# Performance work log

Hardware: AMD Instinct MI355X
Metric: run time of the kernel (lower is better)

Reference implementation:

```python
import jax, jax.numpy as jnp
import numpy as np

B, C, H, W = 64, 32, 112, 112
RANK = 3


def setup_inputs() -> dict:
    key = jax.random.key(0)
    k1, k2, k3, k4, k5 = jax.random.split(key, 5)
    N = H * W  # 12544
    return {
        "x": jax.random.uniform(k1, (B, C, H, W), dtype=jnp.float32),
        "p_buffer": jax.random.normal(k2, (B, N, RANK), dtype=jnp.float32),
        "q_buffer": jax.random.normal(k3, (B, C, RANK), dtype=jnp.float32),
        "grad_p_buffer": jax.random.normal(k4, (B, N, RANK), dtype=jnp.float32),
        "grad_q_buffer": jax.random.normal(k5, (B, C, RANK), dtype=jnp.float32),
        "n_iter": 2,
    }


def _power_svd(X, P, Q, n_iter):
    # X: [b, c, n]; P: [b, n, r]; Q: [b, c, r]
    for i in range(n_iter):
        if i == n_iter - 1:
            P = jnp.linalg.qr(P)[0]  # batched reduced QR, tall-skinny (n x r)
        Q = jnp.einsum('bcn,bnr->bcr', X, P)
        if i == n_iter - 1:
            Q = jnp.linalg.qr(Q)[0]  # batched reduced QR (c x r)
        P = jnp.einsum('bcn,bcr->bnr', X, Q)  # X^T @ Q
    return P, Q


def reference(x, p_buffer, q_buffer, grad_p_buffer, grad_q_buffer, n_iter):
    shape = x.shape
    X = x.reshape(shape[0], shape[1], -1)  # [B, C, H*W]
    P, Q = _power_svd(X, p_buffer, q_buffer, n_iter)
    # low-rank reconstruction Q @ P^T, back to original shape
    return jnp.einsum('bcr,bnr->bcn', Q, P).reshape(shape)
```

## Files before the change

### kernel.cpp

```cpp
#include <hip/hip_runtime.h>
#include <math.h>

#define N_HW 12544
#define TN 128
#define NCH 98
#define KB 16

#define WS_P1 0
#define WS_P2 (64 * KB * 1024)
#define WS_QP (2 * 64 * KB * 1024)
#define WS_U  (WS_QP + 64 * KB * 96)

typedef __attribute__((ext_vector_type(8)))  short short8;
typedef __attribute__((ext_vector_type(16))) float f32x16;
typedef __attribute__((ext_vector_type(4)))  float f32x4;

#define MFMA(a, b, c) __builtin_amdgcn_mfma_f32_32x32x16_bf16((a), (b), (c), 0, 0, 0)

#define LDS_BAR()                                                \
    do {                                                         \
        asm volatile("s_waitcnt lgkmcnt(0)" ::: "memory");       \
        __builtin_amdgcn_s_barrier();                            \
        asm volatile("" ::: "memory");                           \
    } while (0)

__device__ __forceinline__ void split2(float f, ushort& h, ushort& m) {
    unsigned u = __builtin_bit_cast(unsigned, f);
    h = (ushort)(u >> 16);
    float fh = __builtin_bit_cast(float, u & 0xffff0000u);
    float rm = f - fh;
    unsigned um = __builtin_bit_cast(unsigned, rm);
    um += 0x7fffu + ((um >> 16) & 1u);
    m = (ushort)(um >> 16);
}

__device__ __forceinline__ int xq(int c, int o) {
    return c * 16 + ((o & 8) | ((o ^ c) & 7));
}

__global__ __launch_bounds__(256)
void k1_gram(const float* __restrict__ x, const float* __restrict__ p,
             float* __restrict__ P1, float* __restrict__ P2, float* __restrict__ Qp)
{
    const int b = blockIdx.y, kb = blockIdx.x;
    const int tid = threadIdx.x;
    const int lane = tid & 63, wave = tid >> 6;

    __shared__ alignas(16) float SMEM[5120];
    uint4* XS  = (uint4*)SMEM;
    float* dmp = SMEM;
    __shared__ alignas(16) ushort PTH[3 * TN], PTM[3 * TN];

    const int c = tid >> 3, oc = tid & 7;
    const float* xrow = x + ((size_t)b * 32 + c) * N_HW;
    const float* pbat = p + (size_t)b * N_HW * 3;

    f32x16 D1 = {0,0,0,0,0,0,0,0,0,0,0,0,0,0,0,0};
    f32x16 D2 = {0,0,0,0,0,0,0,0,0,0,0,0,0,0,0,0};
    f32x16 DQ = {0,0,0,0,0,0,0,0,0,0,0,0,0,0,0,0};
    const int cl = lane & 31, g = lane >> 5;
    const int rr = (cl < 3) ? cl : 0;

#define LOADX(PX, jj)                                                          \
    do {                                                                       \
        const float4* xr = (const float4*)(xrow + (size_t)(jj) * TN);          \
        PX[0] = xr[2 * oc];      PX[1] = xr[2 * oc + 1];                       \
        PX[2] = xr[2 * oc + 16]; PX[3] = xr[2 * oc + 17];                      \
    } while (0)

#define LOADP(PP, jj)                                                          \
    do { if (tid < TN) {                                                       \
        const float* pb = pbat + (size_t)((jj) * TN + tid) * 3;                \
        PP[0] = pb[0]; PP[1] = pb[1]; PP[2] = pb[2];                           \
    } } while (0)

#define STAGE(PX, PP)                                                          \
    do {                                                                       \
        _Pragma("unroll")                                                      \
        for (int t = 0; t < 2; ++t) {                                          \
            const int o = oc + 8 * t;                                          \
            float4 f0 = PX[2 * t], f1 = PX[2 * t + 1];                         \
            float fv[8] = {f0.x, f0.y, f0.z, f0.w, f1.x, f1.y, f1.z, f1.w};    \
            unsigned hw[4], mw[4];                                             \
            _Pragma("unroll")                                                  \
            for (int i = 0; i < 4; ++i) {                                      \
                ushort h0, m0, h1, m1;                                         \
                split2(fv[2 * i],     h0, m0);                                 \
                split2(fv[2 * i + 1], h1, m1);                                 \
                hw[i] = (unsigned)h0 | ((unsigned)h1 << 16);                   \
                mw[i] = (unsigned)m0 | ((unsigned)m1 << 16);                   \
            }                                                                  \
            const int s = xq(c, o);                                            \
            XS[s]       = make_uint4(hw[0], hw[1], hw[2], hw[3]);              \
            XS[512 + s] = make_uint4(mw[0], mw[1], mw[2], mw[3]);              \
        }                                                                      \
        if (tid < TN) {                                                        \
            _Pragma("unroll")                                                  \
            for (int r = 0; r < 3; ++r) {                                      \
                ushort h, m;                                                   \
                split2(PP[r], h, m);                                           \
                PTH[r * TN + tid] = h; PTM[r * TN + tid] = m;                  \
            }                                                                  \
        }                                                                      \
    } while (0)

#define MFMA_PHASE()                                                           \
    do {                                                                       \
        __builtin_amdgcn_s_setprio(1);                                         \
        for (int s = wave; s < 8; s += 4) {                                    \
            const int sl = xq(cl, 2 * s + g);                                  \
            short8 xh = __builtin_bit_cast(short8, XS[sl]);                    \
            short8 xm = __builtin_bit_cast(short8, XS[512 + sl]);              \
            const int po = rr * TN + 16 * s + 8 * g;                           \
            short8 ph = *(const short8*)&PTH[po];                              \
            short8 pm = *(const short8*)&PTM[po];                              \
            D1 = MFMA(xh, xh, D1);                                             \
            D1 = MFMA(xm, xm, D1);                                             \
            D2 = MFMA(xh, xm, D2);                                             \
            DQ = MFMA(xh, ph, DQ);                                             \
            DQ = MFMA(xm, ph, DQ);                                             \
            DQ = MFMA(xh, pm, DQ);                                             \
            DQ = MFMA(xm, pm, DQ);                                             \
        }                                                                      \
        __builtin_amdgcn_s_setprio(0);                                         \
    } while (0)

    float4 XA[4], XB[4];
    float  PA[3], PB[3];
    int j = kb, jB = kb + KB;
    LOADX(XA, j); LOADP(PA, j);
    bool hasB = (jB < NCH);
    if (hasB) { LOADX(XB, jB); LOADP(PB, jB); }

    while (true) {
        STAGE(XA, PA);
        const int jn = j + 2 * KB;
        const bool preA = (jn < NCH);
        if (preA) { LOADX(XA, jn); LOADP(PA, jn); }
        LDS_BAR();
        MFMA_PHASE();
        if (!hasB) break;
        LDS_BAR();

        STAGE(XB, PB);
        const int jn2 = jB + 2 * KB;
        const bool preB = (jn2 < NCH);
        if (preB) { LOADX(XB, jn2); LOADP(PB, jn2); }
        LDS_BAR();
        MFMA_PHASE();
        if (!preA) break;
        LDS_BAR();

        j = jn; jB = jn2; hasB = preB;
    }

    #define DUMP_REDUCE_G(D, gdst)                                                         \
        __syncthreads();                                                                   \
        _Pragma("unroll")                                                                  \
        for (int i = 0; i < 4; ++i)                                                        \
            *(float4*)&dmp[tid * 20 + 4 * i] =                                             \
                make_float4((D)[4*i], (D)[4*i+1], (D)[4*i+2], (D)[4*i+3]);                 \
        __syncthreads();                                                                   \
        _Pragma("unroll")                                                                  \
        for (int it = 0; it < 4; ++it) {                                                   \
            const int e = tid + 256 * it;                                                  \
            const int r = e >> 5, co = e & 31;                                             \
            const int ln = co + 32 * ((r >> 2) & 1);                                       \
            const int rg = (r & 3) + 4 * (r >> 3);                                         \
            (gdst)[e] = dmp[ln * 20 + rg] + dmp[(64 + ln) * 20 + rg]                       \
                      + dmp[(128 + ln) * 20 + rg] + dmp[(192 + ln) * 20 + rg];             \
        }

    float* p1 = P1 + ((size_t)b * KB + kb) * 1024;
    float* p2 = P2 + ((size_t)b * KB + kb) * 1024;
    DUMP_REDUCE_G(D1, p1)
    DUMP_REDUCE_G(D2, p2)

    __syncthreads();
    #pragma unroll
    for (int i = 0; i < 4; ++i)
        *(float4*)&dmp[tid * 20 + 4 * i] = make_float4(DQ[4*i], DQ[4*i+1], DQ[4*i+2], DQ[4*i+3]);
    __syncthreads();
    if (tid < 96) {
        const int c2 = tid / 3, r2 = tid - 3 * c2;
        const int ln = r2 + 32 * ((c2 >> 2) & 1);
        const int rg = (c2 & 3) + 4 * (c2 >> 3);
        float s = dmp[ln * 20 + rg] + dmp[(64 + ln) * 20 + rg]
                + dmp[(128 + ln) * 20 + rg] + dmp[(192 + ln) * 20 + rg];
        Qp[((size_t)b * KB + kb) * 96 + tid] = s;
    }
}

__global__ __launch_bounds__(256)
void k2_solve(const float* __restrict__ P1, const float* __restrict__ P2,
              const float* __restrict__ Qp, float* __restrict__ Uo)
{
    const int b = blockIdx.x, tid = threadIdx.x;
    __shared__ float S[1024], A2[1024];
    __shared__ float Qv[96], V[96], G[6], L[6];

    f32x4 a1 = {0.f, 0.f, 0.f, 0.f}, a2 = {0.f, 0.f, 0.f, 0.f};
    const float4* p1 = (const float4*)(P1 + (size_t)b * KB * 1024);
    const float4* p2 = (const float4*)(P2 + (size_t)b * KB * 1024);
    #pragma unroll 4
    for (int kb = 0; kb < KB; ++kb) {
        float4 v1 = p1[kb * 256 + tid];
        float4 v2 = p2[kb * 256 + tid];
        a1.x += v1.x; a1.y += v1.y; a1.z += v1.z; a1.w += v1.w;
        a2.x += v2.x; a2.y += v2.y; a2.z += v2.z; a2.w += v2.w;
    }
    A2[4 * tid + 0] = a2.x; A2[4 * tid + 1] = a2.y;
    A2[4 * tid + 2] = a2.z; A2[4 * tid + 3] = a2.w;
    if (tid < 96) {
        const float* qp = Qp + (size_t)b * KB * 96;
        float q = 0.f;
        #pragma unroll 4
        for (int kb = 0; kb < KB; ++kb) q += qp[kb * 96 + tid];
        Qv[tid] = q;
    }
    __syncthreads();
    #pragma unroll
    for (int i = 0; i < 4; ++i) {
        const int e = 4 * tid + i;
        const int et = ((e & 31) << 5) | (e >> 5);
        S[e] = ((i == 0) ? a1.x : (i == 1) ? a1.y : (i == 2) ? a1.z : a1.w)
             + ((i == 0) ? a2.x : (i == 1) ? a2.y : (i == 2) ? a2.z : a2.w)
             + A2[et];
    }
    __syncthreads();

    if (tid < 96) {
        const int c = tid / 3, r = tid % 3;
        float s = 0.f;
        #pragma unroll 8
        for (int cc = 0; cc < 32; ++cc) s += S[c * 32 + cc] * Qv[cc * 3 + r];
        V[tid] = s;
    }
    for (int round = 0; round < 2; ++round) {
        __syncthreads();
        if (tid < 6) {
            const int r = (tid > 2) ? 2 : ((tid > 0) ? 1 : 0);
            const int s = tid - (r * (r + 1)) / 2;
            float g = 0.f;
            for (int c = 0; c < 32; ++c) g += V[c * 3 + r] * V[c * 3 + s];
            G[tid] = g;
        }
        __syncthreads();
        if (tid == 0) {
            const float l00 = sqrtf(G[0]);
            const float l10 = G[1] / l00, l20 = G[3] / l00;
            const float l11 = sqrtf(G[2] - l10 * l10);
            const float l21 = (G[4] - l20 * l10) / l11;
            const float l22 = sqrtf(G[5] - l20 * l20 - l21 * l21);
            L[0] = l00; L[1] = l10; L[2] = l11; L[3] = l20; L[4] = l21; L[5] = l22;
        }
        __syncthreads();
        if (tid < 32) {
            const float v0 = V[tid * 3 + 0], v1 = V[tid * 3 + 1], v2 = V[tid * 3 + 2];
            const float u0 = v0 / L[0];
            const float u1 = (v1 - L[1] * u0) / L[2];
            const float u2 = (v2 - L[3] * u0 - L[4] * u1) / L[5];
            V[tid * 3 + 0] = u0; V[tid * 3 + 1] = u1; V[tid * 3 + 2] = u2;
        }
    }
    __syncthreads();
    if (tid < 32) {
        Uo[(size_t)b * 128 + tid * 4 + 0] = V[tid * 3 + 0];
        Uo[(size_t)b * 128 + tid * 4 + 1] = V[tid * 3 + 1];
        Uo[(size_t)b * 128 + tid * 4 + 2] = V[tid * 3 + 2];
        Uo[(size_t)b * 128 + tid * 4 + 3] = 0.f;
    }
}

__global__ __launch_bounds__(256)
void k3_out(const float* __restrict__ x, const float* __restrict__ Uw,
            float* __restrict__ out)
{
    const int b = blockIdx.y, tid = threadIdx.x;
    __shared__ float Us[32][4];
    if (tid < 128) ((float*)Us)[tid] = Uw[(size_t)b * 128 + tid];
    __syncthreads();
    const int g = blockIdx.x * 256 + tid;
    if (g >= N_HW / 4) return;

    const float* Xb = x   + (size_t)b * 32 * N_HW + 4 * (size_t)g;
    float*       Ob = out + (size_t)b * 32 * N_HW + 4 * (size_t)g;

    float t0x = 0, t0y = 0, t0z = 0, t0w = 0;
    float t1x = 0, t1y = 0, t1z = 0, t1w = 0;
    float t2x = 0, t2y = 0, t2z = 0, t2w = 0;
    #pragma unroll 16
    for (int c = 0; c < 32; ++c) {
        float4 xv = *(const float4*)(Xb + (size_t)c * N_HW);
        const float u0 = Us[c][0], u1 = Us[c][1], u2 = Us[c][2];
        t0x += u0 * xv.x; t0y += u0 * xv.y; t0z += u0 * xv.z; t0w += u0 * xv.w;
        t1x += u1 * xv.x; t1y += u1 * xv.y; t1z += u1 * xv.z; t1w += u1 * xv.w;
        t2x += u2 * xv.x; t2y += u2 * xv.y; t2z += u2 * xv.z; t2w += u2 * xv.w;
    }
    #pragma unroll 16
    for (int c = 0; c < 32; ++c) {
        const float u0 = Us[c][0], u1 = Us[c][1], u2 = Us[c][2];
        f32x4 o;
        o.x = u0 * t0x + u1 * t1x + u2 * t2x;
        o.y = u0 * t0y + u1 * t1y + u2 * t2y;
        o.z = u0 * t0z + u1 * t1z + u2 * t2z;
        o.w = u0 * t0w + u1 * t1w + u2 * t2w;
        __builtin_nontemporal_store(o, (f32x4*)(Ob + (size_t)c * N_HW));
    }
}

extern "C" void kernel_launch(void* const* d_in, const int* in_sizes, int n_in,
                              void* d_out, int out_size, void* d_ws, size_t ws_size,
                              hipStream_t stream)
{
    const float* x = (const float*)d_in[0];
    const float* p = (const float*)d_in[1];
    float* ws = (float*)d_ws;
    float* P1 = ws + WS_P1;
    float* P2 = ws + WS_P2;
    float* Qp = ws + WS_QP;
    float* U  = ws + WS_U;
    float* out = (float*)d_out;

    hipLaunchKernelGGL(k1_gram, dim3(KB, 64), dim3(256), 0, stream, x, p, P1, P2, Qp);
    hipLaunchKernelGGL(k2_solve, dim3(64), dim3(256), 0, stream, P1, P2, Qp, U);
    hipLaunchKernelGGL(k3_out, dim3((N_HW / 4 + 255) / 256, 64), dim3(256), 0, stream, x, U, out);
}
```

Baseline: 226.9 us.

## Fuse gram, solve and output kernels into one cooperative kernel with grid syncs

```diff
diff --git a/kernel.cpp b/kernel.cpp
--- a/kernel.cpp
+++ b/kernel.cpp
@@ -1,15 +1,23 @@
 #include <hip/hip_runtime.h>
+#include <hip/hip_cooperative_groups.h>
 #include <math.h>
+
+namespace cg = cooperative_groups;
 
 #define N_HW 12544
 #define TN 128
 #define NCH 98
-#define KB 16
-
-#define WS_P1 0
-#define WS_P2 (64 * KB * 1024)
-#define WS_QP (2 * 64 * KB * 1024)
-#define WS_U  (WS_QP + 64 * KB * 96)
+#define NB 64
+#define KBF 8
+#define NG4 392
+#define KBB 16
+
+#define FP2 (NB * KBF * 1024)
+#define FQP (2 * NB * KBF * 1024)
+#define FU  (FQP + NB * KBF * 96)
+#define BP2 (NB * KBB * 1024)
+#define BQP (2 * NB * KBB * 1024)
+#define BU  (BQP + NB * KBB * 96)
 
 typedef __attribute__((ext_vector_type(8)))  short short8;
 typedef __attribute__((ext_vector_type(16))) float f32x16;
@@ -38,28 +46,12 @@
     return c * 16 + ((o & 8) | ((o ^ c) & 7));
 }
 
-__global__ __launch_bounds__(256)
-void k1_gram(const float* __restrict__ x, const float* __restrict__ p,
-             float* __restrict__ P1, float* __restrict__ P2, float* __restrict__ Qp)
-{
-    const int b = blockIdx.y, kb = blockIdx.x;
-    const int tid = threadIdx.x;
-    const int lane = tid & 63, wave = tid >> 6;
-
-    __shared__ alignas(16) float SMEM[5120];
-    uint4* XS  = (uint4*)SMEM;
-    float* dmp = SMEM;
-    __shared__ alignas(16) ushort PTH[3 * TN], PTM[3 * TN];
-
-    const int c = tid >> 3, oc = tid & 7;
-    const float* xrow = x + ((size_t)b * 32 + c) * N_HW;
-    const float* pbat = p + (size_t)b * N_HW * 3;
-
-    f32x16 D1 = {0,0,0,0,0,0,0,0,0,0,0,0,0,0,0,0};
-    f32x16 D2 = {0,0,0,0,0,0,0,0,0,0,0,0,0,0,0,0};
-    f32x16 DQ = {0,0,0,0,0,0,0,0,0,0,0,0,0,0,0,0};
-    const int cl = lane & 31, g = lane >> 5;
-    const int rr = (cl < 3) ? cl : 0;
+__device__ __forceinline__ float agent_ld(const float* p) {
+    return __hip_atomic_load((float*)p, __ATOMIC_RELAXED, __HIP_MEMORY_SCOPE_AGENT);
+}
+__device__ __forceinline__ void agent_st(float* p, float v) {
+    __hip_atomic_store(p, v, __ATOMIC_RELAXED, __HIP_MEMORY_SCOPE_AGENT);
+}
 
 #define LOADX(PX, jj)                                                          \
     do {                                                                       \
@@ -125,16 +117,250 @@
         __builtin_amdgcn_s_setprio(0);                                         \
     } while (0)
 
+#define DUMP_REDUCE_G(D, gdst)                                                         \
+    __syncthreads();                                                                   \
+    _Pragma("unroll")                                                                  \
+    for (int i = 0; i < 4; ++i)                                                        \
+        *(float4*)&dmp[tid * 20 + 4 * i] =                                             \
+            make_float4((D)[4*i], (D)[4*i+1], (D)[4*i+2], (D)[4*i+3]);                 \
+    __syncthreads();                                                                   \
+    _Pragma("unroll")                                                                  \
+    for (int it = 0; it < 4; ++it) {                                                   \
+        const int e = tid + 256 * it;                                                  \
+        const int r = e >> 5, co = e & 31;                                             \
+        const int ln = co + 32 * ((r >> 2) & 1);                                       \
+        const int rg = (r & 3) + 4 * (r >> 3);                                         \
+        (gdst)[e] = dmp[ln * 20 + rg] + dmp[(64 + ln) * 20 + rg]                       \
+                  + dmp[(128 + ln) * 20 + rg] + dmp[(192 + ln) * 20 + rg];             \
+    }
+
+#define DUMP_Q(Qdst)                                                                   \
+    __syncthreads();                                                                   \
+    _Pragma("unroll")                                                                  \
+    for (int i = 0; i < 4; ++i)                                                        \
+        *(float4*)&dmp[tid * 20 + 4 * i] = make_float4(DQ[4*i], DQ[4*i+1], DQ[4*i+2], DQ[4*i+3]); \
+    __syncthreads();                                                                   \
+    if (tid < 96) {                                                                    \
+        const int c2 = tid / 3, r2 = tid - 3 * c2;                                     \
+        const int ln = r2 + 32 * ((c2 >> 2) & 1);                                      \
+        const int rg = (c2 & 3) + 4 * (c2 >> 3);                                       \
+        float s = dmp[ln * 20 + rg] + dmp[(64 + ln) * 20 + rg]                         \
+                + dmp[(128 + ln) * 20 + rg] + dmp[(192 + ln) * 20 + rg];               \
+        (Qdst)[tid] = s;                                                               \
+    }
+
+__global__ __launch_bounds__(256, 2)
+void k_fused(const float* __restrict__ x, const float* __restrict__ p,
+             float* __restrict__ P1, float* __restrict__ P2, float* __restrict__ Qp,
+             float* __restrict__ U, float* __restrict__ out)
+{
+    const int bid = blockIdx.x;
+    const int b = bid >> 3, kb = bid & 7;
+    const int tid = threadIdx.x;
+    const int lane = tid & 63, wave = tid >> 6;
+
+    __shared__ alignas(16) float SMEM[5120];
+    uint4* XS  = (uint4*)SMEM;
+    float* dmp = SMEM;
+    __shared__ alignas(16) ushort PTH[3 * TN], PTM[3 * TN];
+    __shared__ float Us[32][4];
+
+    {
+        const int c = tid >> 3, oc = tid & 7;
+        const float* xrow = x + ((size_t)b * 32 + c) * N_HW;
+        const float* pbat = p + (size_t)b * N_HW * 3;
+
+        f32x16 D1 = {0,0,0,0,0,0,0,0,0,0,0,0,0,0,0,0};
+        f32x16 D2 = {0,0,0,0,0,0,0,0,0,0,0,0,0,0,0,0};
+        f32x16 DQ = {0,0,0,0,0,0,0,0,0,0,0,0,0,0,0,0};
+        const int cl = lane & 31, g = lane >> 5;
+        const int rr = (cl < 3) ? cl : 0;
+
+        float4 XA[4], XB[4];
+        float  PA[3], PB[3];
+        int j = kb, jB = kb + KBF;
+        LOADX(XA, j); LOADP(PA, j);
+        bool hasB = (jB < NCH);
+        if (hasB) { LOADX(XB, jB); LOADP(PB, jB); }
+
+        while (true) {
+            STAGE(XA, PA);
+            const int jn = j + 2 * KBF;
+            const bool preA = (jn < NCH);
+            if (preA) { LOADX(XA, jn); LOADP(PA, jn); }
+            LDS_BAR();
+            MFMA_PHASE();
+            if (!hasB) break;
+            LDS_BAR();
+
+            STAGE(XB, PB);
+            const int jn2 = jB + 2 * KBF;
+            const bool preB = (jn2 < NCH);
+            if (preB) { LOADX(XB, jn2); LOADP(PB, jn2); }
+            LDS_BAR();
+            MFMA_PHASE();
+            if (!preA) break;
+            LDS_BAR();
+
+            j = jn; jB = jn2; hasB = preB;
+        }
+
+        float* p1 = P1 + ((size_t)b * KBF + kb) * 1024;
+        float* p2 = P2 + ((size_t)b * KBF + kb) * 1024;
+        DUMP_REDUCE_G(D1, p1)
+        DUMP_REDUCE_G(D2, p2)
+        DUMP_Q(Qp + ((size_t)b * KBF + kb) * 96)
+    }
+
+    __threadfence();
+    cg::this_grid().sync();
+
+    if (kb == 0) {
+        float* S  = SMEM;
+        float* A2 = SMEM + 1024;
+        float* Qv = SMEM + 2048;
+        float* V  = SMEM + 2176;
+        float* G  = SMEM + 2304;
+        float* L  = SMEM + 2312;
+
+        float a1[4] = {0.f, 0.f, 0.f, 0.f}, a2[4] = {0.f, 0.f, 0.f, 0.f};
+        const float* p1 = P1 + (size_t)b * KBF * 1024;
+        const float* p2 = P2 + (size_t)b * KBF * 1024;
+        #pragma unroll
+        for (int kk = 0; kk < KBF; ++kk) {
+            #pragma unroll
+            for (int i = 0; i < 4; ++i) {
+                a1[i] += agent_ld(p1 + kk * 1024 + 4 * tid + i);
+                a2[i] += agent_ld(p2 + kk * 1024 + 4 * tid + i);
+            }
+        }
+        #pragma unroll
+        for (int i = 0; i < 4; ++i) A2[4 * tid + i] = a2[i];
+        if (tid < 96) {
+            const float* qp = Qp + (size_t)b * KBF * 96;
+            float q = 0.f;
+            #pragma unroll
+            for (int kk = 0; kk < KBF; ++kk) q += agent_ld(qp + kk * 96 + tid);
+            Qv[tid] = q;
+        }
+        __syncthreads();
+        #pragma unroll
+        for (int i = 0; i < 4; ++i) {
+            const int e = 4 * tid + i;
+            const int et = ((e & 31) << 5) | (e >> 5);
+            S[e] = a1[i] + a2[i] + A2[et];
+        }
+        __syncthreads();
+
+        if (tid < 96) {
+            const int cc = tid / 3, r = tid % 3;
+            float s = 0.f;
+            #pragma unroll 8
+            for (int c2 = 0; c2 < 32; ++c2) s += S[cc * 32 + c2] * Qv[c2 * 3 + r];
+            V[tid] = s;
+        }
+        for (int round = 0; round < 2; ++round) {
+            __syncthreads();
+            if (tid < 6) {
+                const int r = (tid > 2) ? 2 : ((tid > 0) ? 1 : 0);
+                const int s = tid - (r * (r + 1)) / 2;
+                float gsum = 0.f;
+                for (int c2 = 0; c2 < 32; ++c2) gsum += V[c2 * 3 + r] * V[c2 * 3 + s];
+                G[tid] = gsum;
+            }
+            __syncthreads();
+            if (tid == 0) {
+                const float l00 = sqrtf(G[0]);
+                const float l10 = G[1] / l00, l20 = G[3] / l00;
+                const float l11 = sqrtf(G[2] - l10 * l10);
+                const float l21 = (G[4] - l20 * l10) / l11;
+                const float l22 = sqrtf(G[5] - l20 * l20 - l21 * l21);
+                L[0] = l00; L[1] = l10; L[2] = l11; L[3] = l20; L[4] = l21; L[5] = l22;
+            }
+            __syncthreads();
+            if (tid < 32) {
+                const float v0 = V[tid * 3 + 0], v1 = V[tid * 3 + 1], v2 = V[tid * 3 + 2];
+                const float u0 = v0 / L[0];
+                const float u1 = (v1 - L[1] * u0) / L[2];
+                const float u2 = (v2 - L[3] * u0 - L[4] * u1) / L[5];
+                V[tid * 3 + 0] = u0; V[tid * 3 + 1] = u1; V[tid * 3 + 2] = u2;
+            }
+        }
+        __syncthreads();
+        if (tid < 128) {
+            const int cc = tid >> 2, r = tid & 3;
+            agent_st(U + (size_t)b * 128 + tid, (r < 3) ? V[cc * 3 + r] : 0.f);
+        }
+    }
+
+    __threadfence();
+    cg::this_grid().sync();
+
+    if (tid < 128) ((float*)Us)[tid] = agent_ld(U + (size_t)b * 128 + tid);
+    __syncthreads();
+    {
+        const float* Xb = x   + (size_t)b * 32 * N_HW;
+        float*       Ob = out + (size_t)b * 32 * N_HW;
+        for (int gg = tid; gg < NG4; gg += 256) {
+            const size_t off = (size_t)4 * (kb * NG4 + gg);
+            float t0x = 0, t0y = 0, t0z = 0, t0w = 0;
+            float t1x = 0, t1y = 0, t1z = 0, t1w = 0;
+            float t2x = 0, t2y = 0, t2z = 0, t2w = 0;
+            #pragma unroll 16
+            for (int c = 0; c < 32; ++c) {
+                float4 xv = *(const float4*)(Xb + (size_t)c * N_HW + off);
+                const float u0 = Us[c][0], u1 = Us[c][1], u2 = Us[c][2];
+                t0x += u0 * xv.x; t0y += u0 * xv.y; t0z += u0 * xv.z; t0w += u0 * xv.w;
+                t1x += u1 * xv.x; t1y += u1 * xv.y; t1z += u1 * xv.z; t1w += u1 * xv.w;
+                t2x += u2 * xv.x; t2y += u2 * xv.y; t2z += u2 * xv.z; t2w += u2 * xv.w;
+            }
+            #pragma unroll 16
+            for (int c = 0; c < 32; ++c) {
+                const float u0 = Us[c][0], u1 = Us[c][1], u2 = Us[c][2];
+                f32x4 o;
+                o.x = u0 * t0x + u1 * t1x + u2 * t2x;
+                o.y = u0 * t0y + u1 * t1y + u2 * t2y;
+                o.z = u0 * t0z + u1 * t1z + u2 * t2z;
+                o.w = u0 * t0w + u1 * t1w + u2 * t2w;
+                __builtin_nontemporal_store(o, (f32x4*)(Ob + (size_t)c * N_HW + off));
+            }
+        }
+    }
+}
+
+__global__ __launch_bounds__(256)
+void fb_k1(const float* __restrict__ x, const float* __restrict__ p,
+           float* __restrict__ P1, float* __restrict__ P2, float* __restrict__ Qp)
+{
+    const int b = blockIdx.y, kb = blockIdx.x;
+    const int tid = threadIdx.x;
+    const int lane = tid & 63, wave = tid >> 6;
+
+    __shared__ alignas(16) float SMEM[5120];
+    uint4* XS  = (uint4*)SMEM;
+    float* dmp = SMEM;
+    __shared__ alignas(16) ushort PTH[3 * TN], PTM[3 * TN];
+
+    const int c = tid >> 3, oc = tid & 7;
+    const float* xrow = x + ((size_t)b * 32 + c) * N_HW;
+    const float* pbat = p + (size_t)b * N_HW * 3;
+
+    f32x16 D1 = {0,0,0,0,0,0,0,0,0,0,0,0,0,0,0,0};
+    f32x16 D2 = {0,0,0,0,0,0,0,0,0,0,0,0,0,0,0,0};
+    f32x16 DQ = {0,0,0,0,0,0,0,0,0,0,0,0,0,0,0,0};
+    const int cl = lane & 31, g = lane >> 5;
+    const int rr = (cl < 3) ? cl : 0;
+
     float4 XA[4], XB[4];
     float  PA[3], PB[3];
-    int j = kb, jB = kb + KB;
+    int j = kb, jB = kb + KBB;
     LOADX(XA, j); LOADP(PA, j);
     bool hasB = (jB < NCH);
     if (hasB) { LOADX(XB, jB); LOADP(PB, jB); }
 
     while (true) {
         STAGE(XA, PA);
-        const int jn = j + 2 * KB;
+        const int jn = j + 2 * KBB;
         const bool preA = (jn < NCH);
         if (preA) { LOADX(XA, jn); LOADP(PA, jn); }
         LDS_BAR();
@@ -143,7 +369,7 @@
         LDS_BAR();
 
         STAGE(XB, PB);
-        const int jn2 = jB + 2 * KB;
+        const int jn2 = jB + 2 * KBB;
         const bool preB = (jn2 < NCH);
         if (preB) { LOADX(XB, jn2); LOADP(PB, jn2); }
         LDS_BAR();
@@ -154,56 +380,26 @@
         j = jn; jB = jn2; hasB = preB;
     }
 
-    #define DUMP_REDUCE_G(D, gdst)                                                         \
-        __syncthreads();                                                                   \
-        _Pragma("unroll")                                                                  \
-        for (int i = 0; i < 4; ++i)                                                        \
-            *(float4*)&dmp[tid * 20 + 4 * i] =                                             \
-                make_float4((D)[4*i], (D)[4*i+1], (D)[4*i+2], (D)[4*i+3]);                 \
-        __syncthreads();                                                                   \
-        _Pragma("unroll")                                                                  \
-        for (int it = 0; it < 4; ++it) {                                                   \
-            const int e = tid + 256 * it;                                                  \
-            const int r = e >> 5, co = e & 31;                                             \
-            const int ln = co + 32 * ((r >> 2) & 1);                                       \
-            const int rg = (r & 3) + 4 * (r >> 3);                                         \
-            (gdst)[e] = dmp[ln * 20 + rg] + dmp[(64 + ln) * 20 + rg]                       \
-                      + dmp[(128 + ln) * 20 + rg] + dmp[(192 + ln) * 20 + rg];             \
-        }
-
-    float* p1 = P1 + ((size_t)b * KB + kb) * 1024;
-    float* p2 = P2 + ((size_t)b * KB + kb) * 1024;
+    float* p1 = P1 + ((size_t)b * KBB + kb) * 1024;
+    float* p2 = P2 + ((size_t)b * KBB + kb) * 1024;
     DUMP_REDUCE_G(D1, p1)
     DUMP_REDUCE_G(D2, p2)
-
-    __syncthreads();
-    #pragma unroll
-    for (int i = 0; i < 4; ++i)
-        *(float4*)&dmp[tid * 20 + 4 * i] = make_float4(DQ[4*i], DQ[4*i+1], DQ[4*i+2], DQ[4*i+3]);
-    __syncthreads();
-    if (tid < 96) {
-        const int c2 = tid / 3, r2 = tid - 3 * c2;
-        const int ln = r2 + 32 * ((c2 >> 2) & 1);
-        const int rg = (c2 & 3) + 4 * (c2 >> 3);
-        float s = dmp[ln * 20 + rg] + dmp[(64 + ln) * 20 + rg]
-                + dmp[(128 + ln) * 20 + rg] + dmp[(192 + ln) * 20 + rg];
-        Qp[((size_t)b * KB + kb) * 96 + tid] = s;
-    }
+    DUMP_Q(Qp + ((size_t)b * KBB + kb) * 96)
 }
 
 __global__ __launch_bounds__(256)
-void k2_solve(const float* __restrict__ P1, const float* __restrict__ P2,
-              const float* __restrict__ Qp, float* __restrict__ Uo)
+void fb_k2(const float* __restrict__ P1, const float* __restrict__ P2,
+           const float* __restrict__ Qp, float* __restrict__ Uo)
 {
     const int b = blockIdx.x, tid = threadIdx.x;
     __shared__ float S[1024], A2[1024];
     __shared__ float Qv[96], V[96], G[6], L[6];
 
     f32x4 a1 = {0.f, 0.f, 0.f, 0.f}, a2 = {0.f, 0.f, 0.f, 0.f};
-    const float4* p1 = (const float4*)(P1 + (size_t)b * KB * 1024);
-    const float4* p2 = (const float4*)(P2 + (size_t)b * KB * 1024);
+    const float4* p1 = (const float4*)(P1 + (size_t)b * KBB * 1024);
+    const float4* p2 = (const float4*)(P2 + (size_t)b * KBB * 1024);
     #pragma unroll 4
-    for (int kb = 0; kb < KB; ++kb) {
+    for (int kb = 0; kb < KBB; ++kb) {
         float4 v1 = p1[kb * 256 + tid];
         float4 v2 = p2[kb * 256 + tid];
         a1.x += v1.x; a1.y += v1.y; a1.z += v1.z; a1.w += v1.w;
@@ -212,10 +408,10 @@
     A2[4 * tid + 0] = a2.x; A2[4 * tid + 1] = a2.y;
     A2[4 * tid + 2] = a2.z; A2[4 * tid + 3] = a2.w;
     if (tid < 96) {
-        const float* qp = Qp + (size_t)b * KB * 96;
+        const float* qp = Qp + (size_t)b * KBB * 96;
         float q = 0.f;
         #pragma unroll 4
-        for (int kb = 0; kb < KB; ++kb) q += qp[kb * 96 + tid];
+        for (int kb = 0; kb < KBB; ++kb) q += qp[kb * 96 + tid];
         Qv[tid] = q;
     }
     __syncthreads();
@@ -273,8 +469,8 @@
 }
 
 __global__ __launch_bounds__(256)
-void k3_out(const float* __restrict__ x, const float* __restrict__ Uw,
-            float* __restrict__ out)
+void fb_k3(const float* __restrict__ x, const float* __restrict__ Uw,
+           float* __restrict__ out)
 {
     const int b = blockIdx.y, tid = threadIdx.x;
     __shared__ float Us[32][4];
@@ -316,13 +512,25 @@
     const float* x = (const float*)d_in[0];
     const float* p = (const float*)d_in[1];
     float* ws = (float*)d_ws;
-    float* P1 = ws + WS_P1;
-    float* P2 = ws + WS_P2;
-    float* Qp = ws + WS_QP;
-    float* U  = ws + WS_U;
     float* out = (float*)d_out;
 
-    hipLaunchKernelGGL(k1_gram, dim3(KB, 64), dim3(256), 0, stream, x, p, P1, P2, Qp);
-    hipLaunchKernelGGL(k2_solve, dim3(64), dim3(256), 0, stream, P1, P2, Qp, U);
-    hipLaunchKernelGGL(k3_out, dim3((N_HW / 4 + 255) / 256, 64), dim3(256), 0, stream, x, U, out);
-}
+    float* P1 = ws;
+    float* P2 = ws + FP2;
+    float* Qp = ws + FQP;
+    float* U  = ws + FU;
+
+    void* args[] = { (void*)&x, (void*)&p, (void*)&P1, (void*)&P2, (void*)&Qp,
+                     (void*)&U, (void*)&out };
+    hipError_t err = hipLaunchCooperativeKernel((const void*)k_fused, dim3(NB * KBF),
+                                                dim3(256), args, 0, stream);
+    if (err != hipSuccess) {
+        (void)hipGetLastError();
+        float* bP1 = ws;
+        float* bP2 = ws + BP2;
+        float* bQp = ws + BQP;
+        float* bU  = ws + BU;
+        hipLaunchKernelGGL(fb_k1, dim3(KBB, NB), dim3(256), 0, stream, x, p, bP1, bP2, bQp);
+        hipLaunchKernelGGL(fb_k2, dim3(NB), dim3(256), 0, stream, bP1, bP2, bQp, bU);
+        hipLaunchKernelGGL(fb_k3, dim3((N_HW / 4 + 255) / 256, NB), dim3(256), 0, stream, x, bU, out);
+    }
+}
```

New measurement: 442.7 us. 1.95x slower.

## Coalesce X loads and assign contiguous chunk ranges per block with unrolled pipeline

Applied to the files above, without the earlier changes.

```diff
diff --git a/kernel.cpp b/kernel.cpp
--- a/kernel.cpp
+++ b/kernel.cpp
@@ -61,11 +61,14 @@
     const int cl = lane & 31, g = lane >> 5;
     const int rr = (cl < 3) ? cl : 0;
 
+    const int T  = (kb < 2) ? 7 : 6;
+    const int j0 = kb * 6 + ((kb < 2) ? kb : 2);
+
 #define LOADX(PX, jj)                                                          \
     do {                                                                       \
         const float4* xr = (const float4*)(xrow + (size_t)(jj) * TN);          \
-        PX[0] = xr[2 * oc];      PX[1] = xr[2 * oc + 1];                       \
-        PX[2] = xr[2 * oc + 16]; PX[3] = xr[2 * oc + 17];                      \
+        PX[0] = xr[oc];      PX[1] = xr[8 + oc];                               \
+        PX[2] = xr[16 + oc]; PX[3] = xr[24 + oc];                              \
     } while (0)
 
 #define LOADP(PP, jj)                                                          \
@@ -76,23 +79,20 @@
 
 #define STAGE(PX, PP)                                                          \
     do {                                                                       \
+        uint2* XH = (uint2*)XS;                                                \
+        uint2* XM = (uint2*)(XS + 512);                                        \
         _Pragma("unroll")                                                      \
-        for (int t = 0; t < 2; ++t) {                                          \
-            const int o = oc + 8 * t;                                          \
-            float4 f0 = PX[2 * t], f1 = PX[2 * t + 1];                         \
-            float fv[8] = {f0.x, f0.y, f0.z, f0.w, f1.x, f1.y, f1.z, f1.w};    \
-            unsigned hw[4], mw[4];                                             \
-            _Pragma("unroll")                                                  \
-            for (int i = 0; i < 4; ++i) {                                      \
-                ushort h0, m0, h1, m1;                                         \
-                split2(fv[2 * i],     h0, m0);                                 \
-                split2(fv[2 * i + 1], h1, m1);                                 \
-                hw[i] = (unsigned)h0 | ((unsigned)h1 << 16);                   \
-                mw[i] = (unsigned)m0 | ((unsigned)m1 << 16);                   \
-            }                                                                  \
-            const int s = xq(c, o);                                            \
-            XS[s]       = make_uint4(hw[0], hw[1], hw[2], hw[3]);              \
-            XS[512 + s] = make_uint4(mw[0], mw[1], mw[2], mw[3]);              \
+        for (int k = 0; k < 4; ++k) {                                          \
+            float4 f = PX[k];                                                  \
+            ushort h0, m0, h1, m1, h2, m2, h3, m3;                             \
+            split2(f.x, h0, m0); split2(f.y, h1, m1);                          \
+            split2(f.z, h2, m2); split2(f.w, h3, m3);                          \
+            const int o  = 4 * k + (oc >> 1);                                  \
+            const int s2 = xq(c, o) * 2 + (oc & 1);                            \
+            XH[s2] = make_uint2((unsigned)h0 | ((unsigned)h1 << 16),           \
+                                (unsigned)h2 | ((unsigned)h3 << 16));          \
+            XM[s2] = make_uint2((unsigned)m0 | ((unsigned)m1 << 16),           \
+                                (unsigned)m2 | ((unsigned)m3 << 16));          \
         }                                                                      \
         if (tid < TN) {                                                        \
             _Pragma("unroll")                                                  \
@@ -127,32 +127,26 @@
 
     float4 XA[4], XB[4];
     float  PA[3], PB[3];
-    int j = kb, jB = kb + KB;
-    LOADX(XA, j); LOADP(PA, j);
-    bool hasB = (jB < NCH);
-    if (hasB) { LOADX(XB, jB); LOADP(PB, jB); }
-
-    while (true) {
-        STAGE(XA, PA);
-        const int jn = j + 2 * KB;
-        const bool preA = (jn < NCH);
-        if (preA) { LOADX(XA, jn); LOADP(PA, jn); }
-        LDS_BAR();
-        MFMA_PHASE();
-        if (!hasB) break;
-        LDS_BAR();
-
-        STAGE(XB, PB);
-        const int jn2 = jB + 2 * KB;
-        const bool preB = (jn2 < NCH);
-        if (preB) { LOADX(XB, jn2); LOADP(PB, jn2); }
-        LDS_BAR();
-        MFMA_PHASE();
-        if (!preA) break;
-        LDS_BAR();
-
-        j = jn; jB = jn2; hasB = preB;
-    }
+    LOADX(XA, j0);     LOADP(PA, j0);
+    LOADX(XB, j0 + 1); LOADP(PB, j0 + 1);
+
+#define STEP(PX, PP, t)                                                        \
+    if ((t) < T) {                                                             \
+        STAGE(PX, PP);                                                         \
+        const int jp = j0 + (((t) + 2 < T) ? (t) + 2 : T - 1);                 \
+        LOADX(PX, jp); LOADP(PP, jp);                                          \
+        LDS_BAR();                                                             \
+        MFMA_PHASE();                                                          \
+        if ((t) + 1 < T) LDS_BAR();                                            \
+    }
+
+    STEP(XA, PA, 0)
+    STEP(XB, PB, 1)
+    STEP(XA, PA, 2)
+    STEP(XB, PB, 3)
+    STEP(XA, PA, 4)
+    STEP(XB, PB, 5)
+    STEP(XA, PA, 6)
 
     #define DUMP_REDUCE_G(D, gdst)                                                         \
         __syncthreads();                                                                   \
```

Result: no change. 228.0 us (+0.5%).
